# Optimization experiments

Hardware: AMD Instinct MI355X
Metric: run time of the kernel (lower is better)

## Reference

```python
import jax, jax.numpy as jnp
import numpy as np

D_MODEL = 1024
N_HEADS = 16
D_K = D_MODEL // N_HEADS
WINDOW = 512
ROPE_BASE = 10000.0


def _apply_rope(x):
    # x: [B, H, S, D] ; torchtune-style interleaved-pair RoPE
    S, D = x.shape[2], x.shape[3]
    half = D // 2
    inv_freq = 1.0 / (ROPE_BASE ** (jnp.arange(half, dtype=jnp.float32) / half))
    ang = jnp.arange(S, dtype=jnp.float32)[:, None] * inv_freq[None, :]  # [S, half]
    cos = jnp.cos(ang).astype(x.dtype)  # [S, half]
    sin = jnp.sin(ang).astype(x.dtype)
    x_even = x[..., ::2]   # [B,H,S,half]
    x_odd = x[..., 1::2]
    out_even = x_even * cos - x_odd * sin
    out_odd = x_odd * cos + x_even * sin
    return jnp.stack([out_even, out_odd], axis=-1).reshape(x.shape)


def setup_inputs() -> dict:
    key = jax.random.key(0)
    k1, k2, k3 = jax.random.split(key, 3)
    B, S = 2, 2048
    x = jax.random.normal(k1, (B, S, D_MODEL), dtype=jnp.float32)
    # store weights pre-transposed so y = x @ w (same math as nn.Linear)
    w_qkv = jax.random.normal(k2, (D_MODEL, 3 * D_MODEL), dtype=jnp.float32) * (D_MODEL ** -0.5)
    w_o = jax.random.normal(k3, (D_MODEL, D_MODEL), dtype=jnp.float32) * (D_MODEL ** -0.5)
    return {"x": x, "w_qkv": w_qkv, "w_o": w_o}


def reference(x, w_qkv, w_o):
    B, S, _ = x.shape
    qkv = (x @ w_qkv).reshape(B, S, 3, N_HEADS, D_K)
    qkv = jnp.transpose(qkv, (2, 0, 3, 1, 4))  # [3, B, H, S, Dk]
    q, k, v = qkv[0], qkv[1], qkv[2]
    q = _apply_rope(q)
    k = _apply_rope(k)
    # causal sliding-window mask: token i attends to j in [i - WINDOW, i]
    i = jnp.arange(S)[:, None]
    j = jnp.arange(S)[None, :]
    allowed = (j <= i) & (j >= i - WINDOW)
    bias = jnp.where(allowed, 0.0, -jnp.inf).astype(x.dtype)  # [S, S]
    scores = jnp.einsum('bhqd,bhkd->bhqk', q, k) * (D_K ** -0.5) + bias
    attn = jax.nn.softmax(scores, axis=-1)
    out = jnp.einsum('bhqk,bhkd->bhqd', attn, v)  # [B,H,S,Dk]
    out = jnp.transpose(out, (0, 2, 1, 3)).reshape(B, S, D_MODEL)
    return out @ w_o
```

## Files before the change

kernel.cpp:

```cpp
#include <hip/hip_runtime.h>
#include <hip/hip_bf16.h>
#include <math.h>

typedef __bf16 bhalf;
typedef __bf16 bhalf8 __attribute__((ext_vector_type(8)));
typedef float floatx4 __attribute__((ext_vector_type(4)));
typedef _Float16 fh;
typedef _Float16 half2 __attribute__((ext_vector_type(2)));
typedef _Float16 half4 __attribute__((ext_vector_type(4)));

#define MFMA_BF16(A, B, C) __builtin_amdgcn_mfma_f32_16x16x32_bf16((A), (B), (C), 0, 0, 0)
#define MFMA_F16_K16(A, B, C) __builtin_amdgcn_mfma_f32_16x16x16f16((A), (B), (C), 0, 0, 0)

__device__ inline unsigned short bfb(float f) {
  union { bhalf h; unsigned short u; } c;
  c.h = (bhalf)f;
  return c.u;
}
__device__ inline unsigned short fhb(float f) {
  union { fh h; unsigned short u; } c;
  c.h = (fh)f;
  return c.u;
}
__device__ inline half2 cvt_pk_f16(float a, float b) {
  return __builtin_bit_cast(half2, __builtin_amdgcn_cvt_pkrtz(a, b));
}

__device__ inline void gload_lds16(const void* g, void* l) {
  typedef const __attribute__((address_space(1))) unsigned int GU;
  typedef __attribute__((address_space(3))) unsigned int LU;
  __builtin_amdgcn_global_load_lds((GU*)g, (LU*)l, 16, 0, 0);
}

__global__ __launch_bounds__(256) void prep_kernel(const float* __restrict__ x,
                                                   const float* __restrict__ wqkv,
                                                   const float* __restrict__ wo,
                                                   bhalf* __restrict__ x_bf,
                                                   bhalf* __restrict__ wqkvT,
                                                   bhalf* __restrict__ woT) {
  __shared__ float tile[32][33];
  const int bx = blockIdx.x;
  if (bx < 2048) {
    int i = (bx * 256 + threadIdx.x) * 8;
    floatx4 v0 = *(const floatx4*)(x + i);
    floatx4 v1 = *(const floatx4*)(x + i + 4);
    bhalf8 o;
    o[0] = (bhalf)v0[0]; o[1] = (bhalf)v0[1]; o[2] = (bhalf)v0[2]; o[3] = (bhalf)v0[3];
    o[4] = (bhalf)v1[0]; o[5] = (bhalf)v1[1]; o[6] = (bhalf)v1[2]; o[7] = (bhalf)v1[3];
    *(bhalf8*)(x_bf + i) = o;
    return;
  }
  const float* in;
  bhalf* out;
  int C, cx, ry;
  if (bx < 5120) {
    int idx = bx - 2048;
    in = wqkv; out = wqkvT; C = 3072;
    cx = idx % 96; ry = idx / 96;
  } else {
    int idx = bx - 5120;
    in = wo; out = woT; C = 1024;
    cx = idx & 31; ry = idx >> 5;
  }
  const int R = 1024;
  int c0 = cx * 32, r0 = ry * 32;
  int tx = threadIdx.x & 31, ty = threadIdx.x >> 5;
#pragma unroll
  for (int i = 0; i < 32; i += 8)
    tile[ty + i][tx] = in[(size_t)(r0 + ty + i) * C + c0 + tx];
  __syncthreads();
#pragma unroll
  for (int i = 0; i < 32; i += 8)
    out[(size_t)(c0 + ty + i) * R + r0 + tx] = (bhalf)tile[tx][ty + i];
}

__global__ __launch_bounds__(256, 2) void gemm_qkv_kernel(
    const bhalf* __restrict__ A, const bhalf* __restrict__ BT,
    bhalf* __restrict__ qb, bhalf* __restrict__ kb, fh* __restrict__ vb) {
  const int K = 1024;
  __shared__ __attribute__((aligned(16))) bhalf As[128 * 64];
  __shared__ __attribute__((aligned(16))) bhalf Bs[256 * 64];
  const int tid = threadIdx.x;
  const int lane = tid & 63;
  const int w = tid >> 6;
  const int m0 = blockIdx.y * 128, n0 = blockIdx.x * 256;
  const int l15 = lane & 15, lhi = lane >> 4;

  floatx4 acc[8][4];
#pragma unroll
  for (int i = 0; i < 8; ++i)
#pragma unroll
    for (int j = 0; j < 4; ++j) acc[i][j] = (floatx4){0.f, 0.f, 0.f, 0.f};

  const int srow16 = lane >> 2;
  const int scg = (lane & 3) ^ ((lane >> 3) & 3);
  const bhalf* aP0 = A + (size_t)(m0 + 32 * w + srow16) * K + scg * 8;
  const bhalf* aP1 = aP0 + (size_t)16 * K;
  bhalf* aL0 = &As[(2 * w) * 512];
  bhalf* aL1 = &As[(2 * w + 1) * 512];
  const bhalf* bP0 = BT + (size_t)(n0 + 64 * w + srow16) * K + scg * 8;
  const bhalf* bP1 = bP0 + (size_t)16 * K;
  const bhalf* bP2 = bP0 + (size_t)32 * K;
  const bhalf* bP3 = bP0 + (size_t)48 * K;
  bhalf* bL0 = &Bs[(4 * w) * 512];
  bhalf* bL1 = &Bs[(4 * w + 1) * 512];
  bhalf* bL2 = &Bs[(4 * w + 2) * 512];
  bhalf* bL3 = &Bs[(4 * w + 3) * 512];

  const int fro = (l15 * 4 + (lhi ^ ((l15 >> 1) & 3))) * 8;

  for (int k0 = 0; k0 < K; k0 += 64) {
    __syncthreads();
    gload_lds16(aP0 + k0, aL0);
    gload_lds16(aP1 + k0, aL1);
    gload_lds16(bP0 + k0, bL0);
    gload_lds16(bP1 + k0, bL1);
    gload_lds16(bP2 + k0, bL2);
    gload_lds16(bP3 + k0, bL3);
    gload_lds16(aP0 + k0 + 32, aL0 + 4096);
    gload_lds16(aP1 + k0 + 32, aL1 + 4096);
    gload_lds16(bP0 + k0 + 32, bL0 + 8192);
    gload_lds16(bP1 + k0 + 32, bL1 + 8192);
    gload_lds16(bP2 + k0 + 32, bL2 + 8192);
    gload_lds16(bP3 + k0 + 32, bL3 + 8192);
    __syncthreads();
#pragma unroll
    for (int kh = 0; kh < 2; ++kh) {
      bhalf8 af[8], bf[4];
#pragma unroll
      for (int mt = 0; mt < 8; ++mt)
        af[mt] = *(const bhalf8*)&As[kh * 4096 + mt * 512 + fro];
#pragma unroll
      for (int nt = 0; nt < 4; ++nt)
        bf[nt] = *(const bhalf8*)&Bs[kh * 8192 + (4 * w + nt) * 512 + fro];
#pragma unroll
      for (int mt = 0; mt < 8; ++mt)
#pragma unroll
        for (int nt = 0; nt < 4; ++nt)
          acc[mt][nt] = MFMA_BF16(af[mt], bf[nt], acc[mt][nt]);
    }
  }

  const int sel = n0 >> 10;
  if (sel == 2) {
#pragma unroll
    for (int mt = 0; mt < 8; ++mt) {
      int mg = m0 + mt * 16 + lhi * 4;
      int b = mg >> 11, s0 = mg & 2047;
#pragma unroll
      for (int nt = 0; nt < 4; ++nt) {
        int ng = n0 + w * 64 + nt * 16 + l15;
        int h = (ng & 1023) >> 6, d = ng & 63;
        union { unsigned short u[4]; uint2 v2; } pk;
#pragma unroll
        for (int r = 0; r < 4; ++r) pk.u[r] = fhb(acc[mt][nt][r]);
        *(uint2*)&vb[((size_t)((b << 4) + h) * 64 + d) * 2048 + s0] = pk.v2;
      }
    }
  } else {
    bhalf* dst = sel ? kb : qb;
    const float post = sel ? 1.0f : 0.18033688f;
#pragma unroll
    for (int nt = 0; nt < 4; ++nt) {
      int ng = n0 + w * 64 + nt * 16 + l15;
      int h = (ng & 1023) >> 6, d = ng & 63;
      float inv = exp2f((float)(d >> 1) * -0.4152410118609203f);
      float si, ci;
      __sincosf(inv, &si, &ci);
#pragma unroll
      for (int mt = 0; mt < 8; ++mt) {
        int mg = m0 + mt * 16 + lhi * 4;
        int b = mg >> 11, s0 = mg & 2047;
        float sn, cs;
        __sincosf((float)s0 * inv, &sn, &cs);
#pragma unroll
        for (int r = 0; r < 4; ++r) {
          float val = acc[mt][nt][r];
          float partner = __shfl_xor(val, 1, 64);
          if (!(l15 & 1)) {
            float oe = (cs * val - sn * partner) * post;
            float oo = (cs * partner + sn * val) * post;
            unsigned int u = bfb(oe) | ((unsigned int)bfb(oo) << 16);
            *(unsigned int*)&dst[((size_t)((b << 4) + h) * 2048 + (s0 + r)) * 64 + d] = u;
          }
          float cs2 = cs * ci - sn * si;
          sn = sn * ci + cs * si;
          cs = cs2;
        }
      }
    }
  }
}

template <int TN, int SWZ>
__global__ __launch_bounds__(256, 2) void gemm_bt_kernel(
    const bhalf* __restrict__ A, const bhalf* __restrict__ BT, float* __restrict__ Cout,
    int M, int N, int K) {
  constexpr int NT = TN / 32;
  __shared__ __attribute__((aligned(16))) bhalf As[128 * 64];
  __shared__ __attribute__((aligned(16))) bhalf Bs[TN * 64];
  const int tid = threadIdx.x;
  const int lane = tid & 63;
  const int w = tid >> 6, wr = w >> 1, wc = w & 1;

  int m0, n0;
  if constexpr (SWZ) {
    const int nmt = M >> 7;
    const int mchunk = nmt >> 3;
    const int lin = blockIdx.x;
    const int xcd = lin & 7, idx = lin >> 3;
    m0 = (xcd * mchunk + (idx & (mchunk - 1))) * 128;
    n0 = (idx / mchunk) * TN;
  } else {
    m0 = blockIdx.y * 128;
    n0 = blockIdx.x * TN;
  }

  const int l15 = lane & 15, lhi = lane >> 4;

  floatx4 acc[4][NT];
#pragma unroll
  for (int i = 0; i < 4; ++i)
#pragma unroll
    for (int j = 0; j < NT; ++j) acc[i][j] = (floatx4){0.f, 0.f, 0.f, 0.f};

  const int srow16 = lane >> 2;
  const int scg = (lane & 3) ^ ((lane >> 3) & 3);
  const bhalf* aP0 = A + (size_t)(m0 + 32 * w + srow16) * K + scg * 8;
  const bhalf* aP1 = aP0 + (size_t)16 * K;
  const bhalf* bP0 = BT + (size_t)(n0 + 16 * w + srow16) * K + scg * 8;
  bhalf* aL0 = &As[(2 * w) * 512];
  bhalf* aL1 = &As[(2 * w + 1) * 512];
  bhalf* bL0 = &Bs[w * 512];

  const int fro = (l15 * 4 + (lhi ^ ((l15 >> 1) & 3))) * 8;

  for (int k0 = 0; k0 < K; k0 += 64) {
    __syncthreads();
    gload_lds16(aP0 + k0, aL0);
    gload_lds16(aP1 + k0, aL1);
    gload_lds16(bP0 + k0, bL0);
    gload_lds16(aP0 + k0 + 32, aL0 + 4096);
    gload_lds16(aP1 + k0 + 32, aL1 + 4096);
    gload_lds16(bP0 + k0 + 32, bL0 + TN * 32);
    __syncthreads();
#pragma unroll
    for (int kh = 0; kh < 2; ++kh) {
      bhalf8 af[4], bf[NT];
#pragma unroll
      for (int mt = 0; mt < 4; ++mt)
        af[mt] = *(const bhalf8*)&As[kh * 4096 + (wr * 4 + mt) * 512 + fro];
#pragma unroll
      for (int nt = 0; nt < NT; ++nt)
        bf[nt] = *(const bhalf8*)&Bs[kh * TN * 32 + (wc * NT + nt) * 512 + fro];
#pragma unroll
      for (int mt = 0; mt < 4; ++mt)
#pragma unroll
        for (int nt = 0; nt < NT; ++nt)
          acc[mt][nt] = MFMA_BF16(af[mt], bf[nt], acc[mt][nt]);
    }
  }

#pragma unroll
  for (int mt = 0; mt < 4; ++mt)
#pragma unroll
    for (int nt = 0; nt < NT; ++nt)
#pragma unroll
      for (int r = 0; r < 4; ++r) {
        int mg = m0 + wr * 64 + mt * 16 + lhi * 4 + r;
        int ng = n0 + wc * (TN / 2) + nt * 16 + l15;
        Cout[(size_t)mg * N + ng] = acc[mt][nt][r];
      }
}

__global__ __launch_bounds__(256, 2) void attn_kernel(const bhalf* __restrict__ qg,
                                                      const bhalf* __restrict__ kg,
                                                      const fh* __restrict__ vt,
                                                      bhalf* __restrict__ attn_out) {
  __shared__ __attribute__((aligned(16))) bhalf Ks[4][8 * 512];
  __shared__ __attribute__((aligned(16))) fh Vs[4][16 * 256];

  const int lin = blockIdx.x;
  const int xcd = lin & 7, idx = lin >> 3;
  const int bh = xcd * 4 + (idx & 3);
  const int qt2 = idx >> 2;

  const int tid = threadIdx.x, lane = tid & 63, w = tid >> 6;
  const int l15 = lane & 15, quad = lane >> 4;
  const int q0 = qt2 * 128;
  const int qtile0 = qt2 * 2;
  const size_t base = (size_t)bh * 2048 * 64;
  const size_t vbase = (size_t)bh * 64 * 2048;

  bhalf8 qa[2][2];
#pragma unroll
  for (int h = 0; h < 2; ++h) {
    const bhalf* qp = qg + base + (size_t)(q0 + h * 64 + w * 16 + l15) * 64 + quad * 8;
    qa[h][0] = *(const bhalf8*)qp;
    qa[h][1] = *(const bhalf8*)(qp + 32);
  }

  const int kOff = (w * 16 + (lane >> 2)) * 64 + (lane & 3) * 8;
  const int vfb0 = 4 * w + (lane >> 5), vfb1 = 4 * w + 2 + (lane >> 5);
  const int vOff0 = ((vfb0 & 3) * 16 + ((lane & 31) >> 1)) * 2048 + w * 16 + (lane & 1) * 8;
  const int vOff1 = ((vfb1 & 3) * 16 + ((lane & 31) >> 1)) * 2048 + w * 16 + (lane & 1) * 8;

  floatx4 O[2][4];
#pragma unroll
  for (int h = 0; h < 2; ++h)
#pragma unroll
    for (int dt = 0; dt < 4; ++dt) O[h][dt] = (floatx4){0.f, 0.f, 0.f, 0.f};
  float lsum[2] = {0.f, 0.f};

  auto stage = [&](int kt, int buf) {
    const bhalf* kp = kg + base + (size_t)(kt * 64) * 64 + kOff;
    gload_lds16(kp, &Ks[buf][(2 * w) * 512]);
    gload_lds16(kp + 32, &Ks[buf][(2 * w + 1) * 512]);
    const fh* vp = vt + vbase + kt * 64;
    gload_lds16(vp + vOff0, &Vs[buf][(2 * w) * 512]);
    gload_lds16(vp + vOff1, &Vs[buf][(2 * w + 1) * 512]);
  };

  auto proc2 = [&](int buf, int kt) {
    const bool va = (kt <= qtile0) && (kt >= qtile0 - 8);
    const bool vb_ = (kt <= qtile0 + 1) && (kt >= qtile0 - 7);
    floatx4 sf[2][4];
    __builtin_amdgcn_s_setprio(1);
#pragma unroll
    for (int nt = 0; nt < 4; ++nt) {
      bhalf8 k0 = *(const bhalf8*)&Ks[buf][(nt * 2) * 512 + (l15 * 4 + quad) * 8];
      bhalf8 k1 = *(const bhalf8*)&Ks[buf][(nt * 2 + 1) * 512 + (l15 * 4 + quad) * 8];
      floatx4 s0 = (floatx4){0.f, 0.f, 0.f, 0.f};
      floatx4 s1 = (floatx4){0.f, 0.f, 0.f, 0.f};
      if (va) {
        s0 = MFMA_BF16(k0, qa[0][0], s0);
        s0 = MFMA_BF16(k1, qa[0][1], s0);
      }
      if (vb_) {
        s1 = MFMA_BF16(k0, qa[1][0], s1);
        s1 = MFMA_BF16(k1, qa[1][1], s1);
      }
      sf[0][nt] = s0;
      sf[1][nt] = s1;
    }
    __builtin_amdgcn_s_setprio(0);

    half4 pf[2][4];
#pragma unroll
    for (int h = 0; h < 2; ++h) {
      if (!(h == 0 ? va : vb_)) continue;
      const int diag = qtile0 + h;
      const int iG = q0 + h * 64 + w * 16 + l15;
      if (kt == diag) {
#pragma unroll
        for (int nt = 0; nt < 4; ++nt) {
          int jb = kt * 64 + nt * 16 + quad * 4;
#pragma unroll
          for (int r = 0; r < 4; ++r)
            if (jb + r > iG) sf[h][nt][r] = -1e30f;
        }
      } else if (kt == diag - 8) {
#pragma unroll
        for (int nt = 0; nt < 4; ++nt) {
          int jb = kt * 64 + nt * 16 + quad * 4;
#pragma unroll
          for (int r = 0; r < 4; ++r)
            if (jb + r + 512 < iG) sf[h][nt][r] = -1e30f;
        }
      }
#pragma unroll
      for (int nt = 0; nt < 4; ++nt) {
        float p0 = exp2f(sf[h][nt][0]);
        float p1 = exp2f(sf[h][nt][1]);
        float p2 = exp2f(sf[h][nt][2]);
        float p3 = exp2f(sf[h][nt][3]);
        lsum[h] += (p0 + p1) + (p2 + p3);
        union { half2 h2[2]; half4 h4; } pu;
        pu.h2[0] = cvt_pk_f16(p0, p1);
        pu.h2[1] = cvt_pk_f16(p2, p3);
        pf[h][nt] = pu.h4;
      }
    }

    __builtin_amdgcn_s_setprio(1);
#pragma unroll
    for (int nt = 0; nt < 4; ++nt) {
#pragma unroll
      for (int dt = 0; dt < 4; ++dt) {
        half4 vf = *(const half4*)&Vs[buf][(nt * 4 + dt) * 256 + (l15 * 4 + quad) * 4];
        if (va) O[0][dt] = MFMA_F16_K16(vf, pf[0][nt], O[0][dt]);
        if (vb_) O[1][dt] = MFMA_F16_K16(vf, pf[1][nt], O[1][dt]);
      }
    }
    __builtin_amdgcn_s_setprio(0);
  };

  int ktstart = qtile0 - 8;
  if (ktstart < 0) ktstart = 0;
  const int ktend = qtile0 + 1;
  const int ntot = ktend - ktstart + 1;

  stage(ktstart, 0);
  stage(ktstart + 1, 1);
  __syncthreads();

  for (int i = 0; i < ntot; ++i) {
    const int kt = ktstart + i;
    if (i + 2 < ntot) {
      stage(kt + 2, (i + 2) & 3);
      asm volatile("s_waitcnt vmcnt(8)" ::: "memory");
    } else if (i + 2 == ntot) {
      asm volatile("s_waitcnt vmcnt(4)" ::: "memory");
    } else {
      asm volatile("s_waitcnt vmcnt(0)" ::: "memory");
    }
    __builtin_amdgcn_s_barrier();
    proc2(i & 3, kt);
  }

  const int b = bh >> 4, hh = bh & 15;
#pragma unroll
  for (int h = 0; h < 2; ++h) {
    float t = lsum[h];
    t += __shfl_xor(t, 16, 64);
    t += __shfl_xor(t, 32, 64);
    const float inv = 1.f / t;
    const int s = q0 + h * 64 + w * 16 + l15;
#pragma unroll
    for (int dt = 0; dt < 4; ++dt) {
      union { unsigned short u[4]; uint2 v2; } pk;
#pragma unroll
      for (int r = 0; r < 4; ++r) pk.u[r] = bfb(O[h][dt][r] * inv);
      *(uint2*)&attn_out[(size_t)(b * 2048 + s) * 1024 + hh * 64 + dt * 16 + quad * 4] = pk.v2;
    }
  }
}

extern "C" void kernel_launch(void* const* d_in, const int* in_sizes, int n_in,
                              void* d_out, int out_size, void* d_ws, size_t ws_size,
                              hipStream_t stream) {
  (void)in_sizes; (void)n_in; (void)out_size; (void)ws_size;
  const float* x = (const float*)d_in[0];
  const float* w_qkv = (const float*)d_in[1];
  const float* w_o = (const float*)d_in[2];
  float* out = (float*)d_out;
  char* ws = (char*)d_ws;

  bhalf* x_bf  = (bhalf*)(ws);
  bhalf* wqkvT = (bhalf*)(ws + ((size_t)8 << 20));
  bhalf* woT   = (bhalf*)(ws + ((size_t)14 << 20));
  bhalf* qb    = (bhalf*)(ws + ((size_t)16 << 20));
  bhalf* kb    = (bhalf*)(ws + ((size_t)24 << 20));
  fh*    vb    = (fh*)(ws + ((size_t)32 << 20));
  bhalf* attn  = (bhalf*)(ws + ((size_t)40 << 20));

  prep_kernel<<<6144, 256, 0, stream>>>(x, w_qkv, w_o, x_bf, wqkvT, woT);
  gemm_qkv_kernel<<<dim3(12, 32), 256, 0, stream>>>(x_bf, wqkvT, qb, kb, vb);
  attn_kernel<<<512, 256, 0, stream>>>(qb, kb, vb, attn);
  gemm_bt_kernel<64, 1><<<512, 256, 0, stream>>>(attn, woT, out, 4096, 1024, 1024);
}
```

Measured before the change: 170.0 us.

## Rewrite QKV GEMM as 256x256 8-wave double-buffered pipelined kernel

Replaces the 128x256 four-wave QKV GEMM with a 256x256 tile using eight waves in a 2x4 grid. LDS is double-buffered, and the next K-slice's global-to-LDS loads are interleaved between MFMA phases, using explicit vmcnt waits, barriers and s_setprio. This is meant to overlap memory latency with matrix math and halve the block count. The RoPE epilogue now advances sin/cos by rotation across row tiles instead of calling sincos per tile. Costs are one block per CU, higher register pressure and more barriers. The SWZ template parameter of the output GEMM is also folded away.

```diff
diff --git a/kernel.cpp b/kernel.cpp
--- a/kernel.cpp
+++ b/kernel.cpp
@@ -74,82 +74,123 @@
     out[(size_t)(c0 + ty + i) * R + r0 + tx] = (bhalf)tile[tx][ty + i];
 }
 
-__global__ __launch_bounds__(256, 2) void gemm_qkv_kernel(
+__global__ __launch_bounds__(512, 1) void gemm_qkv8_kernel(
     const bhalf* __restrict__ A, const bhalf* __restrict__ BT,
     bhalf* __restrict__ qb, bhalf* __restrict__ kb, fh* __restrict__ vb) {
   const int K = 1024;
-  __shared__ __attribute__((aligned(16))) bhalf As[128 * 64];
-  __shared__ __attribute__((aligned(16))) bhalf Bs[256 * 64];
-  const int tid = threadIdx.x;
-  const int lane = tid & 63;
-  const int w = tid >> 6;
-  const int m0 = blockIdx.y * 128, n0 = blockIdx.x * 256;
+  __shared__ __attribute__((aligned(16))) bhalf As[2][16384];
+  __shared__ __attribute__((aligned(16))) bhalf Bs[2][16384];
+  const int tid = threadIdx.x, lane = tid & 63, w = tid >> 6;
+  const int wr = w >> 2, wc = w & 3;
+  const int m0 = blockIdx.y * 256, n0 = blockIdx.x * 256;
   const int l15 = lane & 15, lhi = lane >> 4;
-
-  floatx4 acc[8][4];
-#pragma unroll
-  for (int i = 0; i < 8; ++i)
-#pragma unroll
-    for (int j = 0; j < 4; ++j) acc[i][j] = (floatx4){0.f, 0.f, 0.f, 0.f};
-
   const int srow16 = lane >> 2;
   const int scg = (lane & 3) ^ ((lane >> 3) & 3);
   const bhalf* aP0 = A + (size_t)(m0 + 32 * w + srow16) * K + scg * 8;
   const bhalf* aP1 = aP0 + (size_t)16 * K;
-  bhalf* aL0 = &As[(2 * w) * 512];
-  bhalf* aL1 = &As[(2 * w + 1) * 512];
-  const bhalf* bP0 = BT + (size_t)(n0 + 64 * w + srow16) * K + scg * 8;
+  const bhalf* bP0 = BT + (size_t)(n0 + 32 * w + srow16) * K + scg * 8;
   const bhalf* bP1 = bP0 + (size_t)16 * K;
-  const bhalf* bP2 = bP0 + (size_t)32 * K;
-  const bhalf* bP3 = bP0 + (size_t)48 * K;
-  bhalf* bL0 = &Bs[(4 * w) * 512];
-  bhalf* bL1 = &Bs[(4 * w + 1) * 512];
-  bhalf* bL2 = &Bs[(4 * w + 2) * 512];
-  bhalf* bL3 = &Bs[(4 * w + 3) * 512];
-
   const int fro = (l15 * 4 + (lhi ^ ((l15 >> 1) & 3))) * 8;
 
-  for (int k0 = 0; k0 < K; k0 += 64) {
-    __syncthreads();
-    gload_lds16(aP0 + k0, aL0);
-    gload_lds16(aP1 + k0, aL1);
-    gload_lds16(bP0 + k0, bL0);
-    gload_lds16(bP1 + k0, bL1);
-    gload_lds16(bP2 + k0, bL2);
-    gload_lds16(bP3 + k0, bL3);
-    gload_lds16(aP0 + k0 + 32, aL0 + 4096);
-    gload_lds16(aP1 + k0 + 32, aL1 + 4096);
-    gload_lds16(bP0 + k0 + 32, bL0 + 8192);
-    gload_lds16(bP1 + k0 + 32, bL1 + 8192);
-    gload_lds16(bP2 + k0 + 32, bL2 + 8192);
-    gload_lds16(bP3 + k0 + 32, bL3 + 8192);
-    __syncthreads();
-#pragma unroll
-    for (int kh = 0; kh < 2; ++kh) {
-      bhalf8 af[8], bf[4];
-#pragma unroll
-      for (int mt = 0; mt < 8; ++mt)
-        af[mt] = *(const bhalf8*)&As[kh * 4096 + mt * 512 + fro];
+  floatx4 acc[8][4];
+#pragma unroll
+  for (int i = 0; i < 8; ++i)
+#pragma unroll
+    for (int j = 0; j < 4; ++j) acc[i][j] = (floatx4){0.f, 0.f, 0.f, 0.f};
+
+  auto stageA = [&](int k0, int buf, int kh) {
+    gload_lds16(aP0 + k0 + kh * 32, &As[buf][kh * 8192 + (2 * w) * 512]);
+    gload_lds16(aP1 + k0 + kh * 32, &As[buf][kh * 8192 + (2 * w + 1) * 512]);
+  };
+  auto stageB = [&](int k0, int buf, int kh) {
+    gload_lds16(bP0 + k0 + kh * 32, &Bs[buf][kh * 8192 + (2 * w) * 512]);
+    gload_lds16(bP1 + k0 + kh * 32, &Bs[buf][kh * 8192 + (2 * w + 1) * 512]);
+  };
+
+  stageA(0, 0, 0); stageA(0, 0, 1); stageB(0, 0, 0); stageB(0, 0, 1);
+  __syncthreads();
+
+  for (int t = 0; t < 16; ++t) {
+    const int k0 = t * 64;
+    const int buf = t & 1, nb = buf ^ 1;
+    const bool pf = (t < 15);
+    bhalf8 af[4], bf[4];
+
+    if (pf) {
+      stageA(k0 + 64, nb, 0);
+      asm volatile("s_waitcnt vmcnt(2)" ::: "memory");
+    } else {
+      asm volatile("s_waitcnt vmcnt(0)" ::: "memory");
+    }
+    __builtin_amdgcn_s_barrier();
+    asm volatile("" ::: "memory");
+#pragma unroll
+    for (int mt = 0; mt < 4; ++mt)
+      af[mt] = *(const bhalf8*)&As[buf][(wr * 8 + mt) * 512 + fro];
+#pragma unroll
+    for (int nt = 0; nt < 4; ++nt)
+      bf[nt] = *(const bhalf8*)&Bs[buf][(wc * 4 + nt) * 512 + fro];
+    __builtin_amdgcn_s_setprio(1);
+#pragma unroll
+    for (int mt = 0; mt < 4; ++mt)
 #pragma unroll
       for (int nt = 0; nt < 4; ++nt)
-        bf[nt] = *(const bhalf8*)&Bs[kh * 8192 + (4 * w + nt) * 512 + fro];
-#pragma unroll
-      for (int mt = 0; mt < 8; ++mt)
-#pragma unroll
-        for (int nt = 0; nt < 4; ++nt)
-          acc[mt][nt] = MFMA_BF16(af[mt], bf[nt], acc[mt][nt]);
-    }
-  }
-
-  const int sel = n0 >> 10;
+        acc[mt][nt] = MFMA_BF16(af[mt], bf[nt], acc[mt][nt]);
+    __builtin_amdgcn_s_setprio(0);
+    __builtin_amdgcn_s_barrier();
+
+    if (pf) stageB(k0 + 64, nb, 0);
+#pragma unroll
+    for (int mt = 0; mt < 4; ++mt)
+      af[mt] = *(const bhalf8*)&As[buf][(wr * 8 + 4 + mt) * 512 + fro];
+    __builtin_amdgcn_s_setprio(1);
+#pragma unroll
+    for (int mt = 0; mt < 4; ++mt)
+#pragma unroll
+      for (int nt = 0; nt < 4; ++nt)
+        acc[4 + mt][nt] = MFMA_BF16(af[mt], bf[nt], acc[4 + mt][nt]);
+    __builtin_amdgcn_s_setprio(0);
+    __builtin_amdgcn_s_barrier();
+
+    if (pf) stageA(k0 + 64, nb, 1);
+#pragma unroll
+    for (int mt = 0; mt < 4; ++mt)
+      af[mt] = *(const bhalf8*)&As[buf][8192 + (wr * 8 + mt) * 512 + fro];
+#pragma unroll
+    for (int nt = 0; nt < 4; ++nt)
+      bf[nt] = *(const bhalf8*)&Bs[buf][8192 + (wc * 4 + nt) * 512 + fro];
+    __builtin_amdgcn_s_setprio(1);
+#pragma unroll
+    for (int mt = 0; mt < 4; ++mt)
+#pragma unroll
+      for (int nt = 0; nt < 4; ++nt)
+        acc[mt][nt] = MFMA_BF16(af[mt], bf[nt], acc[mt][nt]);
+    __builtin_amdgcn_s_setprio(0);
+    __builtin_amdgcn_s_barrier();
+
+    if (pf) stageB(k0 + 64, nb, 1);
+#pragma unroll
+    for (int mt = 0; mt < 4; ++mt)
+      af[mt] = *(const bhalf8*)&As[buf][8192 + (wr * 8 + 4 + mt) * 512 + fro];
+    __builtin_amdgcn_s_setprio(1);
+#pragma unroll
+    for (int mt = 0; mt < 4; ++mt)
+#pragma unroll
+      for (int nt = 0; nt < 4; ++nt)
+        acc[4 + mt][nt] = MFMA_BF16(af[mt], bf[nt], acc[4 + mt][nt]);
+    __builtin_amdgcn_s_setprio(0);
+    __builtin_amdgcn_s_barrier();
+  }
+
+  const int sel = (int)(blockIdx.x >> 2);
   if (sel == 2) {
 #pragma unroll
     for (int mt = 0; mt < 8; ++mt) {
-      int mg = m0 + mt * 16 + lhi * 4;
+      int mg = m0 + wr * 128 + mt * 16 + lhi * 4;
       int b = mg >> 11, s0 = mg & 2047;
 #pragma unroll
       for (int nt = 0; nt < 4; ++nt) {
-        int ng = n0 + w * 64 + nt * 16 + l15;
+        int ng = n0 + wc * 64 + nt * 16 + l15;
         int h = (ng & 1023) >> 6, d = ng & 63;
         union { unsigned short u[4]; uint2 v2; } pk;
 #pragma unroll
@@ -162,17 +203,19 @@
     const float post = sel ? 1.0f : 0.18033688f;
 #pragma unroll
     for (int nt = 0; nt < 4; ++nt) {
-      int ng = n0 + w * 64 + nt * 16 + l15;
+      int ng = n0 + wc * 64 + nt * 16 + l15;
       int h = (ng & 1023) >> 6, d = ng & 63;
       float inv = exp2f((float)(d >> 1) * -0.4152410118609203f);
       float si, ci;
       __sincosf(inv, &si, &ci);
+      float s12, c12;
+      __sincosf(12.f * inv, &s12, &c12);
+      float sn, cs;
+      __sincosf((float)((m0 + wr * 128 + lhi * 4) & 2047) * inv, &sn, &cs);
 #pragma unroll
       for (int mt = 0; mt < 8; ++mt) {
-        int mg = m0 + mt * 16 + lhi * 4;
+        int mg = m0 + wr * 128 + mt * 16 + lhi * 4;
         int b = mg >> 11, s0 = mg & 2047;
-        float sn, cs;
-        __sincosf((float)s0 * inv, &sn, &cs);
 #pragma unroll
         for (int r = 0; r < 4; ++r) {
           float val = acc[mt][nt][r];
@@ -187,12 +230,15 @@
           sn = sn * ci + cs * si;
           cs = cs2;
         }
-      }
-    }
-  }
-}
-
-template <int TN, int SWZ>
+        float cs2 = cs * c12 - sn * s12;
+        sn = sn * c12 + cs * s12;
+        cs = cs2;
+      }
+    }
+  }
+}
+
+template <int TN>
 __global__ __launch_bounds__(256, 2) void gemm_bt_kernel(
     const bhalf* __restrict__ A, const bhalf* __restrict__ BT, float* __restrict__ Cout,
     int M, int N, int K) {
@@ -203,18 +249,12 @@
   const int lane = tid & 63;
   const int w = tid >> 6, wr = w >> 1, wc = w & 1;
 
-  int m0, n0;
-  if constexpr (SWZ) {
-    const int nmt = M >> 7;
-    const int mchunk = nmt >> 3;
-    const int lin = blockIdx.x;
-    const int xcd = lin & 7, idx = lin >> 3;
-    m0 = (xcd * mchunk + (idx & (mchunk - 1))) * 128;
-    n0 = (idx / mchunk) * TN;
-  } else {
-    m0 = blockIdx.y * 128;
-    n0 = blockIdx.x * TN;
-  }
+  const int nmt = M >> 7;
+  const int mchunk = nmt >> 3;
+  const int lin = blockIdx.x;
+  const int xcd = lin & 7, idx = lin >> 3;
+  const int m0 = (xcd * mchunk + (idx & (mchunk - 1))) * 128;
+  const int n0 = (idx / mchunk) * TN;
 
   const int l15 = lane & 15, lhi = lane >> 4;
 
@@ -455,7 +495,7 @@
   bhalf* attn  = (bhalf*)(ws + ((size_t)40 << 20));
 
   prep_kernel<<<6144, 256, 0, stream>>>(x, w_qkv, w_o, x_bf, wqkvT, woT);
-  gemm_qkv_kernel<<<dim3(12, 32), 256, 0, stream>>>(x_bf, wqkvT, qb, kb, vb);
+  gemm_qkv8_kernel<<<dim3(12, 16), 512, 0, stream>>>(x_bf, wqkvT, qb, kb, vb);
   attn_kernel<<<512, 256, 0, stream>>>(qb, kb, vb, attn);
-  gemm_bt_kernel<64, 1><<<512, 256, 0, stream>>>(attn, woT, out, 4096, 1024, 1024);
-}
+  gemm_bt_kernel<64><<<512, 256, 0, stream>>>(attn, woT, out, 4096, 1024, 1024);
+}
```

After: 173.1 us. About the same (+1.8%).
